# Kernel optimization log

Measured on AMD Instinct MI355X. Metric: run time of the kernel, lower is better.

The kernel has to match this reference:

```python
import jax, jax.numpy as jnp
import numpy as np

SLOT_DIM = 256
HIDDEN = 128
NUM_REL = 8


def setup_inputs() -> dict:
    key = jax.random.key(0)
    ks = jax.random.split(key, 5)
    B, N, D = 8, 256, SLOT_DIM
    slots = jax.random.normal(ks[0], (B, N, D), dtype=jnp.float32)
    # Linear(2D -> H): store as [2D, H] (x @ W + b)
    s1 = 1.0 / np.sqrt(2 * D)
    W1 = jax.random.uniform(ks[1], (2 * D, HIDDEN), jnp.float32, -s1, s1)
    b1 = jax.random.uniform(ks[2], (HIDDEN,), jnp.float32, -s1, s1)
    s2 = 1.0 / np.sqrt(HIDDEN)
    W2 = jax.random.uniform(ks[3], (HIDDEN, NUM_REL), jnp.float32, -s2, s2)
    b2 = jax.random.uniform(ks[4], (NUM_REL,), jnp.float32, -s2, s2)
    return {"slots": slots, "W1": W1, "b1": b1, "W2": W2, "b2": b2}


def reference(slots, W1, b1, W2, b2):
    # cat([slots_i, slots_j]) @ W1 == slots_i @ W1[:D] + slots_j @ W1[D:]
    # so project each slot once, then broadcast-add over the pair grid.
    D = slots.shape[-1]
    proj_i = jnp.einsum("bnd,dh->bnh", slots, W1[:D])   # [B,N,H]
    proj_j = jnp.einsum("bnd,dh->bnh", slots, W1[D:])   # [B,N,H]
    h = proj_i[:, :, None, :] + proj_j[:, None, :, :] + b1  # [B,N,N,H]
    h = jax.nn.relu(h)
    logits = jnp.einsum("bijh,hr->bijr", h, W2) + b2     # [B,N,N,R]
    return jax.nn.sigmoid(logits)
```

## Files before the change

kernel.cpp:

```cpp
#include <hip/hip_runtime.h>
#include <hip/hip_fp16.h>
#include <math.h>

#define BATCH 8
#define NSLOT 256
#define DDIM  256
#define HID   128
#define NREL  8

typedef _Float16 half8 __attribute__((ext_vector_type(8)));
typedef float float4v __attribute__((ext_vector_type(4)));

union U8 {
  uint32_t u[4];
  _Float16 f[8];
  half8 v;
  float4 f4;
};

union U4 {
  uint32_t u[2];
  _Float16 f[4];
  uint2 u2;
};


__device__ __forceinline__ int swz(int row, int off) {
  return (off & ~0x70) | ((((off >> 4) ^ row) & 7) << 4);
}

__global__ __launch_bounds__(512, 2) void fused_kernel(
    const float* __restrict__ slots, const float* __restrict__ W1,
    const float* __restrict__ b1, const float* __restrict__ W2,
    const float* __restrict__ b2, float* __restrict__ out) {
  __shared__ _Float16 WuS[128 * 256];
  __shared__ _Float16 SlabS[8][2][16 * 128];
  __shared__ _Float16 PiS[8 * 128];

  const int tid  = threadIdx.x;
  const int w    = tid >> 6;
  const int lane = tid & 63;
  const int lo16 = lane & 15;
  const int kg   = lane >> 4;

  const int b  = blockIdx.y;
  const int i0 = blockIdx.x * 8;
  const float* sb = slots + (size_t)b * NSLOT * DDIM;

  {
    const int c = tid & 127;
    const int kb0 = tid >> 7;
    const float* Wup = W1 + (size_t)DDIM * HID;
#pragma unroll
    for (int s = 0; s < 8; ++s) {
      const int kb = kb0 + s * 4;
      U8 p;
#pragma unroll
      for (int u = 0; u < 8; ++u)
        p.f[u] = (_Float16)Wup[(size_t)(kb * 8 + u) * HID + c];
      *(float4*)((char*)WuS + c * 512 + swz(c, kb * 16)) = p.f4;
    }
  }

  {
    const int c = w * 16 + lo16;
    const float* Wcol = W1 + c;
    U8 bf[8];
#pragma unroll
    for (int ks = 0; ks < 8; ++ks) {
      const int kb = ks * 32 + kg * 8;
#pragma unroll
      for (int u = 0; u < 8; ++u)
        bf[ks].f[u] = (_Float16)Wcol[(size_t)(kb + u) * HID];
    }
    int arow = i0 + lo16;
    if (arow > NSLOT - 1) arow = NSLOT - 1;
    const float* srow = sb + (size_t)arow * DDIM;
    float4v acc = {0.0f, 0.0f, 0.0f, 0.0f};
#pragma unroll
    for (int ks = 0; ks < 8; ++ks) {
      const float4 x0 = *(const float4*)(srow + ks * 32 + kg * 8);
      const float4 x1 = *(const float4*)(srow + ks * 32 + kg * 8 + 4);
      U8 a;
      a.f[0] = (_Float16)x0.x; a.f[1] = (_Float16)x0.y;
      a.f[2] = (_Float16)x0.z; a.f[3] = (_Float16)x0.w;
      a.f[4] = (_Float16)x1.x; a.f[5] = (_Float16)x1.y;
      a.f[6] = (_Float16)x1.z; a.f[7] = (_Float16)x1.w;
      acc = __builtin_amdgcn_mfma_f32_16x16x32_f16(a.v, bf[ks].v, acc, 0, 0, 0);
    }
    const float bias = b1[c];
#pragma unroll
    for (int reg = 0; reg < 4; ++reg) {
      const int m = kg * 4 + reg;
      if (m < 8) PiS[m * 128 + c] = (_Float16)(acc[reg] + bias);
    }
  }

  U8 Bs[2][8];
#pragma unroll
  for (int t = 0; t < 2; ++t) {
    const int j0t = (2 * w + t) * 16;
    const float* srow = sb + (size_t)(j0t + lo16) * DDIM;
#pragma unroll
    for (int ks = 0; ks < 8; ++ks) {
      const float4 x0 = *(const float4*)(srow + ks * 32 + kg * 8);
      const float4 x1 = *(const float4*)(srow + ks * 32 + kg * 8 + 4);
      Bs[t][ks].f[0] = (_Float16)x0.x; Bs[t][ks].f[1] = (_Float16)x0.y;
      Bs[t][ks].f[2] = (_Float16)x0.z; Bs[t][ks].f[3] = (_Float16)x0.w;
      Bs[t][ks].f[4] = (_Float16)x1.x; Bs[t][ks].f[5] = (_Float16)x1.y;
      Bs[t][ks].f[6] = (_Float16)x1.z; Bs[t][ks].f[7] = (_Float16)x1.w;
    }
  }
  U8 w2f[4];
#pragma unroll
  for (int kq = 0; kq < 4; ++kq) {
    const int kb = kq * 32 + kg * 8;
#pragma unroll
    for (int u = 0; u < 8; ++u) {
      const float v = W2[(kb + u) * NREL + (lo16 & 7)];
      w2f[kq].f[u] = (lo16 < NREL) ? (_Float16)v : (_Float16)0.0f;
    }
  }
  const float b2v = (lo16 < NREL) ? b2[lo16 & 7] : 0.0f;

  __syncthreads();

  _Float16* myslab0 = &SlabS[w][0][0];
  _Float16* myslab1 = &SlabS[w][1][0];
#pragma unroll
  for (int ct = 0; ct < 8; ++ct) {
    const int c = ct * 16 + lo16;
    U8 af[8];
#pragma unroll
    for (int ks = 0; ks < 8; ++ks)
      af[ks].f4 = *(const float4*)((const char*)WuS + c * 512 +
                                   swz(c, ks * 64 + kg * 16));
    float4v d0 = {0.0f, 0.0f, 0.0f, 0.0f};
    float4v d1 = {0.0f, 0.0f, 0.0f, 0.0f};
#pragma unroll
    for (int ks = 0; ks < 8; ++ks) {
      d0 = __builtin_amdgcn_mfma_f32_16x16x32_f16(af[ks].v, Bs[0][ks].v, d0, 0, 0, 0);
      d1 = __builtin_amdgcn_mfma_f32_16x16x32_f16(af[ks].v, Bs[1][ks].v, d1, 0, 0, 0);
    }
    U4 s0, s1;
#pragma unroll
    for (int r4 = 0; r4 < 4; ++r4) {
      s0.f[r4] = (_Float16)d0[r4];
      s1.f[r4] = (_Float16)d1[r4];
    }
    const int off = ct * 32 + kg * 8;
    *(uint2*)((char*)myslab0 + lo16 * 256 + swz(lo16, off)) = s0.u2;
    *(uint2*)((char*)myslab1 + lo16 * 256 + swz(lo16, off)) = s1.u2;
  }

  U8 pjf[2][4];
#pragma unroll
  for (int t = 0; t < 2; ++t) {
    const char* base = (const char*)(t ? myslab1 : myslab0);
#pragma unroll
    for (int kq = 0; kq < 4; ++kq)
      pjf[t][kq].f4 = *(const float4*)(base + lo16 * 256 +
                                       swz(lo16, kq * 64 + kg * 16));
  }

#pragma unroll
  for (int i = 0; i < 8; ++i) {
    U8 pif[4];
#pragma unroll
    for (int kq = 0; kq < 4; ++kq)
      pif[kq].f4 = *(const float4*)&PiS[i * 128 + kq * 32 + kg * 8];
#pragma unroll
    for (int t = 0; t < 2; ++t) {
      const int j0t = (2 * w + t) * 16;
      float4v acc = {0.0f, 0.0f, 0.0f, 0.0f};
#pragma unroll
      for (int kq = 0; kq < 4; ++kq) {
        U8 h;
        h.v = __builtin_elementwise_max(pjf[t][kq].v + pif[kq].v,
                                        (half8)(_Float16)0.0f);
        acc = __builtin_amdgcn_mfma_f32_16x16x32_f16(h.v, w2f[kq].v, acc, 0, 0, 0);
      }
      if (lo16 < NREL) {
        float* obase =
            out + (((size_t)b * NSLOT + (i0 + i)) * NSLOT + j0t) * NREL + lo16;
#pragma unroll
        for (int reg = 0; reg < 4; ++reg) {
          const int jrow = kg * 4 + reg;
          const float x = acc[reg] + b2v;
          obase[jrow * NREL] = __builtin_amdgcn_rcpf(1.0f + __expf(-x));
        }
      }
    }
  }
}

extern "C" void kernel_launch(void* const* d_in, const int* in_sizes, int n_in,
                              void* d_out, int out_size, void* d_ws,
                              size_t ws_size, hipStream_t stream) {
  const float* slots = (const float*)d_in[0];
  const float* W1    = (const float*)d_in[1];
  const float* b1    = (const float*)d_in[2];
  const float* W2    = (const float*)d_in[3];
  const float* b2    = (const float*)d_in[4];
  float* out = (float*)d_out;
  (void)d_ws; (void)ws_size;

  fused_kernel<<<dim3(NSLOT / 8, BATCH), 512, 0, stream>>>(slots, W1, b1, W2,
                                                           b2, out);
}
```

Before: 87.36 us.

## Split pair grid into smaller blocks and stream hidden dimension in chunks

The kernel now launches 1024 blocks of 256 threads, each covering 8 i-rows by 64 j-columns, instead of 256 blocks of 512 threads. The hidden dimension is processed in four 32-wide chunks: each chunk stages both halves of W1 into LDS with coalesced float4 loads, computes partial projections, and accumulates the second MLP layer in registers across chunks. This shrinks LDS use and allows more resident blocks, improving occupancy and load balance. The cost is that every block recomputes the W1 conversions and projections, and each chunk adds two block-wide barriers.

```diff
diff --git a/kernel.cpp b/kernel.cpp
--- a/kernel.cpp
+++ b/kernel.cpp
@@ -29,13 +29,14 @@
   return (off & ~0x70) | ((((off >> 4) ^ row) & 7) << 4);
 }
 
-__global__ __launch_bounds__(512, 2) void fused_kernel(
+__global__ __launch_bounds__(256, 4) void fused_kernel(
     const float* __restrict__ slots, const float* __restrict__ W1,
     const float* __restrict__ b1, const float* __restrict__ W2,
     const float* __restrict__ b2, float* __restrict__ out) {
-  __shared__ _Float16 WuS[128 * 256];
-  __shared__ _Float16 SlabS[8][2][16 * 128];
-  __shared__ _Float16 PiS[8 * 128];
+  __shared__ _Float16 WlS[32 * 256];
+  __shared__ _Float16 WuS[32 * 256];
+  __shared__ _Float16 PiS[8 * 32];
+  __shared__ _Float16 SlabS[4][16][40];
 
   const int tid  = threadIdx.x;
   const int w    = tid >> 6;
@@ -43,152 +44,141 @@
   const int lo16 = lane & 15;
   const int kg   = lane >> 4;
 
-  const int b  = blockIdx.y;
-  const int i0 = blockIdx.x * 8;
+  const int bx  = blockIdx.x;
+  const int b   = bx >> 7;
+  const int i0  = ((bx >> 2) & 31) * 8;
+  const int j0w = (bx & 3) * 64 + w * 16;
   const float* sb = slots + (size_t)b * NSLOT * DDIM;
 
+  U8 Bs[8];
   {
-    const int c = tid & 127;
-    const int kb0 = tid >> 7;
-    const float* Wup = W1 + (size_t)DDIM * HID;
-#pragma unroll
-    for (int s = 0; s < 8; ++s) {
-      const int kb = kb0 + s * 4;
-      U8 p;
-#pragma unroll
-      for (int u = 0; u < 8; ++u)
-        p.f[u] = (_Float16)Wup[(size_t)(kb * 8 + u) * HID + c];
-      *(float4*)((char*)WuS + c * 512 + swz(c, kb * 16)) = p.f4;
-    }
-  }
-
-  {
-    const int c = w * 16 + lo16;
-    const float* Wcol = W1 + c;
-    U8 bf[8];
-#pragma unroll
-    for (int ks = 0; ks < 8; ++ks) {
-      const int kb = ks * 32 + kg * 8;
-#pragma unroll
-      for (int u = 0; u < 8; ++u)
-        bf[ks].f[u] = (_Float16)Wcol[(size_t)(kb + u) * HID];
-    }
-    int arow = i0 + lo16;
-    if (arow > NSLOT - 1) arow = NSLOT - 1;
-    const float* srow = sb + (size_t)arow * DDIM;
-    float4v acc = {0.0f, 0.0f, 0.0f, 0.0f};
+    const float* srow = sb + (size_t)(j0w + lo16) * DDIM;
 #pragma unroll
     for (int ks = 0; ks < 8; ++ks) {
       const float4 x0 = *(const float4*)(srow + ks * 32 + kg * 8);
       const float4 x1 = *(const float4*)(srow + ks * 32 + kg * 8 + 4);
-      U8 a;
-      a.f[0] = (_Float16)x0.x; a.f[1] = (_Float16)x0.y;
-      a.f[2] = (_Float16)x0.z; a.f[3] = (_Float16)x0.w;
-      a.f[4] = (_Float16)x1.x; a.f[5] = (_Float16)x1.y;
-      a.f[6] = (_Float16)x1.z; a.f[7] = (_Float16)x1.w;
-      acc = __builtin_amdgcn_mfma_f32_16x16x32_f16(a.v, bf[ks].v, acc, 0, 0, 0);
+      Bs[ks].f[0] = (_Float16)x0.x; Bs[ks].f[1] = (_Float16)x0.y;
+      Bs[ks].f[2] = (_Float16)x0.z; Bs[ks].f[3] = (_Float16)x0.w;
+      Bs[ks].f[4] = (_Float16)x1.x; Bs[ks].f[5] = (_Float16)x1.y;
+      Bs[ks].f[6] = (_Float16)x1.z; Bs[ks].f[7] = (_Float16)x1.w;
     }
-    const float bias = b1[c];
+  }
+  const float b2v = (lo16 < NREL) ? b2[lo16] : 0.0f;
+
+  float4v acc[8];
 #pragma unroll
-    for (int reg = 0; reg < 4; ++reg) {
-      const int m = kg * 4 + reg;
-      if (m < 8) PiS[m * 128 + c] = (_Float16)(acc[reg] + bias);
+  for (int i = 0; i < 8; ++i) acc[i] = (float4v){0.0f, 0.0f, 0.0f, 0.0f};
+
+  for (int kq = 0; kq < 4; ++kq) {
+    {
+      const int kg8 = tid >> 3;
+      const int c4  = (tid & 7) * 4;
+      const int cg  = kq * 32 + c4;
+      float xr[32];
+#pragma unroll
+      for (int u = 0; u < 8; ++u)
+        *(float4*)&xr[u * 4] = *(const float4*)(W1 + (size_t)(kg8 * 8 + u) * HID + cg);
+#pragma unroll
+      for (int j = 0; j < 4; ++j) {
+        U8 p;
+#pragma unroll
+        for (int u = 0; u < 8; ++u) p.f[u] = (_Float16)xr[u * 4 + j];
+        *(float4*)((char*)WlS + (c4 + j) * 512 + swz(c4 + j, kg8 * 16)) = p.f4;
+      }
+#pragma unroll
+      for (int u = 0; u < 8; ++u)
+        *(float4*)&xr[u * 4] =
+            *(const float4*)(W1 + (size_t)(DDIM + kg8 * 8 + u) * HID + cg);
+#pragma unroll
+      for (int j = 0; j < 4; ++j) {
+        U8 p;
+#pragma unroll
+        for (int u = 0; u < 8; ++u) p.f[u] = (_Float16)xr[u * 4 + j];
+        *(float4*)((char*)WuS + (c4 + j) * 512 + swz(c4 + j, kg8 * 16)) = p.f4;
+      }
+    }
+
+    U8 w2s;
+#pragma unroll
+    for (int u = 0; u < 8; ++u) {
+      const float v = W2[(kq * 32 + kg * 8 + u) * NREL + (lo16 & 7)];
+      w2s.f[u] = (lo16 < NREL) ? (_Float16)v : (_Float16)0.0f;
+    }
+
+    __syncthreads();
+
+#pragma unroll
+    for (int ct = 0; ct < 2; ++ct) {
+      const int row = ct * 16 + lo16;
+      U8 af[8];
+#pragma unroll
+      for (int ks = 0; ks < 8; ++ks)
+        af[ks].f4 = *(const float4*)((const char*)WuS + row * 512 +
+                                     swz(row, ks * 64 + kg * 16));
+      float4v d = {0.0f, 0.0f, 0.0f, 0.0f};
+#pragma unroll
+      for (int ks = 0; ks < 8; ++ks)
+        d = __builtin_amdgcn_mfma_f32_16x16x32_f16(af[ks].v, Bs[ks].v, d, 0, 0, 0);
+      U4 s;
+#pragma unroll
+      for (int r = 0; r < 4; ++r) s.f[r] = (_Float16)d[r];
+      *(uint2*)((char*)&SlabS[w][0][0] + lo16 * 80 + ct * 32 + kg * 8) = s.u2;
+    }
+
+    if (w < 2) {
+      const int cl = w * 16 + lo16;
+      U8 bf[8];
+#pragma unroll
+      for (int ks = 0; ks < 8; ++ks)
+        bf[ks].f4 = *(const float4*)((const char*)WlS + cl * 512 +
+                                     swz(cl, ks * 64 + kg * 16));
+      int ar = i0 + lo16;
+      if (ar > NSLOT - 1) ar = NSLOT - 1;
+      const float* srow = sb + (size_t)ar * DDIM;
+      float4v pa = {0.0f, 0.0f, 0.0f, 0.0f};
+#pragma unroll
+      for (int ks = 0; ks < 8; ++ks) {
+        const float4 x0 = *(const float4*)(srow + ks * 32 + kg * 8);
+        const float4 x1 = *(const float4*)(srow + ks * 32 + kg * 8 + 4);
+        U8 a;
+        a.f[0] = (_Float16)x0.x; a.f[1] = (_Float16)x0.y;
+        a.f[2] = (_Float16)x0.z; a.f[3] = (_Float16)x0.w;
+        a.f[4] = (_Float16)x1.x; a.f[5] = (_Float16)x1.y;
+        a.f[6] = (_Float16)x1.z; a.f[7] = (_Float16)x1.w;
+        pa = __builtin_amdgcn_mfma_f32_16x16x32_f16(a.v, bf[ks].v, pa, 0, 0, 0);
+      }
+#pragma unroll
+      for (int reg = 0; reg < 4; ++reg) {
+        const int m = kg * 4 + reg;
+        if (m < 8) PiS[m * 32 + cl] = (_Float16)(pa[reg] + b1[kq * 32 + cl]);
+      }
+    }
+
+    __syncthreads();
+
+    U8 pj;
+    pj.f4 = *(const float4*)((const char*)&SlabS[w][0][0] + lo16 * 80 + kg * 16);
+#pragma unroll
+    for (int i = 0; i < 8; ++i) {
+      U8 pif;
+      pif.f4 = *(const float4*)((const char*)PiS + i * 64 + kg * 16);
+      U8 h;
+      h.v = __builtin_elementwise_max(pj.v + pif.v, (half8)(_Float16)0.0f);
+      acc[i] =
+          __builtin_amdgcn_mfma_f32_16x16x32_f16(h.v, w2s.v, acc[i], 0, 0, 0);
     }
   }
 
-  U8 Bs[2][8];
+  if (lo16 < NREL) {
 #pragma unroll
-  for (int t = 0; t < 2; ++t) {
-    const int j0t = (2 * w + t) * 16;
-    const float* srow = sb + (size_t)(j0t + lo16) * DDIM;
+    for (int i = 0; i < 8; ++i) {
+      float* obase =
+          out + (((size_t)b * NSLOT + (i0 + i)) * NSLOT + j0w) * NREL + lo16;
 #pragma unroll
-    for (int ks = 0; ks < 8; ++ks) {
-      const float4 x0 = *(const float4*)(srow + ks * 32 + kg * 8);
-      const float4 x1 = *(const float4*)(srow + ks * 32 + kg * 8 + 4);
-      Bs[t][ks].f[0] = (_Float16)x0.x; Bs[t][ks].f[1] = (_Float16)x0.y;
-      Bs[t][ks].f[2] = (_Float16)x0.z; Bs[t][ks].f[3] = (_Float16)x0.w;
-      Bs[t][ks].f[4] = (_Float16)x1.x; Bs[t][ks].f[5] = (_Float16)x1.y;
-      Bs[t][ks].f[6] = (_Float16)x1.z; Bs[t][ks].f[7] = (_Float16)x1.w;
-    }
-  }
-  U8 w2f[4];
-#pragma unroll
-  for (int kq = 0; kq < 4; ++kq) {
-    const int kb = kq * 32 + kg * 8;
-#pragma unroll
-    for (int u = 0; u < 8; ++u) {
-      const float v = W2[(kb + u) * NREL + (lo16 & 7)];
-      w2f[kq].f[u] = (lo16 < NREL) ? (_Float16)v : (_Float16)0.0f;
-    }
-  }
-  const float b2v = (lo16 < NREL) ? b2[lo16 & 7] : 0.0f;
-
-  __syncthreads();
-
-  _Float16* myslab0 = &SlabS[w][0][0];
-  _Float16* myslab1 = &SlabS[w][1][0];
-#pragma unroll
-  for (int ct = 0; ct < 8; ++ct) {
-    const int c = ct * 16 + lo16;
-    U8 af[8];
-#pragma unroll
-    for (int ks = 0; ks < 8; ++ks)
-      af[ks].f4 = *(const float4*)((const char*)WuS + c * 512 +
-                                   swz(c, ks * 64 + kg * 16));
-    float4v d0 = {0.0f, 0.0f, 0.0f, 0.0f};
-    float4v d1 = {0.0f, 0.0f, 0.0f, 0.0f};
-#pragma unroll
-    for (int ks = 0; ks < 8; ++ks) {
-      d0 = __builtin_amdgcn_mfma_f32_16x16x32_f16(af[ks].v, Bs[0][ks].v, d0, 0, 0, 0);
-      d1 = __builtin_amdgcn_mfma_f32_16x16x32_f16(af[ks].v, Bs[1][ks].v, d1, 0, 0, 0);
-    }
-    U4 s0, s1;
-#pragma unroll
-    for (int r4 = 0; r4 < 4; ++r4) {
-      s0.f[r4] = (_Float16)d0[r4];
-      s1.f[r4] = (_Float16)d1[r4];
-    }
-    const int off = ct * 32 + kg * 8;
-    *(uint2*)((char*)myslab0 + lo16 * 256 + swz(lo16, off)) = s0.u2;
-    *(uint2*)((char*)myslab1 + lo16 * 256 + swz(lo16, off)) = s1.u2;
-  }
-
-  U8 pjf[2][4];
-#pragma unroll
-  for (int t = 0; t < 2; ++t) {
-    const char* base = (const char*)(t ? myslab1 : myslab0);
-#pragma unroll
-    for (int kq = 0; kq < 4; ++kq)
-      pjf[t][kq].f4 = *(const float4*)(base + lo16 * 256 +
-                                       swz(lo16, kq * 64 + kg * 16));
-  }
-
-#pragma unroll
-  for (int i = 0; i < 8; ++i) {
-    U8 pif[4];
-#pragma unroll
-    for (int kq = 0; kq < 4; ++kq)
-      pif[kq].f4 = *(const float4*)&PiS[i * 128 + kq * 32 + kg * 8];
-#pragma unroll
-    for (int t = 0; t < 2; ++t) {
-      const int j0t = (2 * w + t) * 16;
-      float4v acc = {0.0f, 0.0f, 0.0f, 0.0f};
-#pragma unroll
-      for (int kq = 0; kq < 4; ++kq) {
-        U8 h;
-        h.v = __builtin_elementwise_max(pjf[t][kq].v + pif[kq].v,
-                                        (half8)(_Float16)0.0f);
-        acc = __builtin_amdgcn_mfma_f32_16x16x32_f16(h.v, w2f[kq].v, acc, 0, 0, 0);
-      }
-      if (lo16 < NREL) {
-        float* obase =
-            out + (((size_t)b * NSLOT + (i0 + i)) * NSLOT + j0t) * NREL + lo16;
-#pragma unroll
-        for (int reg = 0; reg < 4; ++reg) {
-          const int jrow = kg * 4 + reg;
-          const float x = acc[reg] + b2v;
-          obase[jrow * NREL] = __builtin_amdgcn_rcpf(1.0f + __expf(-x));
-        }
+      for (int reg = 0; reg < 4; ++reg) {
+        const int jrow = kg * 4 + reg;
+        const float x = acc[i][reg] + b2v;
+        obase[jrow * NREL] = __builtin_amdgcn_rcpf(1.0f + __expf(-x));
       }
     }
   }
@@ -205,6 +195,5 @@
   float* out = (float*)d_out;
   (void)d_ws; (void)ws_size;
 
-  fused_kernel<<<dim3(NSLOT / 8, BATCH), 512, 0, stream>>>(slots, W1, b1, W2,
-                                                           b2, out);
+  fused_kernel<<<dim3(1024), 256, 0, stream>>>(slots, W1, b1, W2, b2, out);
 }
```

New measurement: 125.8 us. 44.0% more time.
